# Performance work log

Measured on AMD Instinct MI355X. Metric: run time of the kernel, lower is better.

The kernel has to match this reference:

```python
import jax, jax.numpy as jnp
import numpy as np

NUM_GRAPHS = 512
LEAKY_SLOPE = 0.01


def _gconv(x, src, dst, w, W_root, W_rel, b_rel):
    # PyG GraphConv: out = lin_rel(sum_j w_ij * x_j) + lin_root(x)
    msg = x[src] * w[:, None]                       # [E, d] gather + scale
    agg = jax.ops.segment_sum(msg, dst, num_segments=x.shape[0])  # scatter-add
    return agg @ W_rel + b_rel + x @ W_root


def setup_inputs() -> dict:
    key = jax.random.key(0)
    ks = jax.random.split(key, 12)
    N, E, D, H, C = 100000, 1250000, 64, 64, 8
    x_embeddings = jax.random.normal(ks[0], (N, D), dtype=jnp.float32)
    edge_index = jax.random.randint(ks[1], (2, E), 0, N, dtype=jnp.int64)
    weights = jax.random.uniform(ks[2], (E,), dtype=jnp.float32)
    batch = jnp.sort(jax.random.randint(ks[3], (N,), 0, NUM_GRAPHS, dtype=jnp.int64))
    s1 = 1.0 / np.sqrt(D)
    s2 = 1.0 / np.sqrt(H)
    W1_root = jax.random.uniform(ks[4], (D, H), jnp.float32, -s1, s1)
    W1_rel = jax.random.uniform(ks[5], (D, H), jnp.float32, -s1, s1)
    b1 = jax.random.uniform(ks[6], (H,), jnp.float32, -s1, s1)
    W2_root = jax.random.uniform(ks[7], (H, H), jnp.float32, -s2, s2)
    W2_rel = jax.random.uniform(ks[8], (H, H), jnp.float32, -s2, s2)
    b2 = jax.random.uniform(ks[9], (H,), jnp.float32, -s2, s2)
    Wl_root = jax.random.uniform(ks[10], (H, C), jnp.float32, -s2, s2)
    bl = jax.random.uniform(ks[11], (C,), jnp.float32, -s2, s2)
    return {"x_embeddings": x_embeddings, "edge_index": edge_index,
            "weights": weights, "batch": batch,
            "W1_root": W1_root, "W1_rel": W1_rel, "b1": b1,
            "W2_root": W2_root, "W2_rel": W2_rel, "b2": b2,
            "Wl_root": Wl_root, "bl": bl}


def reference(x_embeddings, edge_index, weights, batch,
              W1_root, W1_rel, b1, W2_root, W2_rel, b2, Wl_root, bl):
    src, dst = edge_index[0], edge_index[1]
    x = _gconv(x_embeddings, src, dst, weights, W1_root, W1_rel, b1)
    x = jax.nn.leaky_relu(x, LEAKY_SLOPE)
    x = _gconv(x, src, dst, weights, W2_root, W2_rel, b2)
    x = jax.nn.leaky_relu(x, LEAKY_SLOPE)
    # global_mean_pool over graph ids
    summed = jax.ops.segment_sum(x, batch, num_segments=NUM_GRAPHS)
    counts = jax.ops.segment_sum(jnp.ones((x.shape[0],), x.dtype), batch,
                                 num_segments=NUM_GRAPHS)
    pooled = summed / jnp.maximum(counts, 1.0)[:, None]
    # final GraphConv applied with no edges: agg = 0 -> W_root x + b_rel
    out = pooled @ Wl_root + bl
    return out
```

## Files before the change

kernel.cpp:

```cpp
#include <hip/hip_runtime.h>

#define LEAKY_SLOPE 0.01f
#define NUM_GRAPHS 512
#define TILE 4096
#define NB_MAX 512
#define POOL_SPAN 8

typedef __attribute__((ext_vector_type(8))) short short8;
typedef __attribute__((ext_vector_type(4))) float f32x4;

static __device__ __forceinline__ unsigned short f2bf(float f) {
    unsigned u = __float_as_uint(f);
    u += 0x7FFFu + ((u >> 16) & 1u);
    return (unsigned short)(u >> 16);
}
static __device__ __forceinline__ float bf2f(unsigned short h) {
    return __uint_as_float(((unsigned)h) << 16);
}

static __device__ __forceinline__ int wave_incl_scan(int v, int lane) {
#pragma unroll
    for (int off = 1; off < 64; off <<= 1) {
        int t = __shfl_up(v, off, 64);
        if (lane >= off) v += t;
    }
    return v;
}

__global__ __launch_bounds__(256)
void hist_kernel(const int* __restrict__ dst, int* __restrict__ bucketCnt,
                 int E, int NB) {
    __shared__ int h[NB_MAX];
    for (int t = threadIdx.x; t < NB_MAX; t += 256) h[t] = 0;
    __syncthreads();
    const int base = blockIdx.x * TILE;
#pragma unroll
    for (int i = 0; i < TILE / 256; ++i) {
        int e = base + i * 256 + threadIdx.x;
        if (e < E) atomicAdd(&h[dst[e] >> 8], 1);
    }
    __syncthreads();
    for (int t = threadIdx.x; t < NB; t += 256)
        if (h[t]) atomicAdd(&bucketCnt[t], h[t]);
}

__global__ __launch_bounds__(512)
void bscan_kernel(const int* __restrict__ bucketCnt, int* __restrict__ bucketBase,
                  int* __restrict__ cursor, int* __restrict__ rowStart,
                  float* __restrict__ pooled, int N, int E, int NB) {
    __shared__ int ws[8];
    const int t = threadIdx.x, lane = t & 63, wid = t >> 6;
    int v = (t < NB) ? bucketCnt[t] : 0;
    int s = wave_incl_scan(v, lane);
    if (lane == 63) ws[wid] = s;
    __syncthreads();
    int add = 0;
    for (int i = 0; i < wid; ++i) add += ws[i];
    if (t < NB) {
        int excl = s + add - v;
        bucketBase[t] = excl;
        cursor[t] = excl;
    }
    if (t == 0) rowStart[N] = E;
    float4 z = make_float4(0.f, 0.f, 0.f, 0.f);
#pragma unroll
    for (int i = 0; i < 16; ++i)
        ((float4*)pooled)[t * 16 + i] = z;
}

__global__ __launch_bounds__(256)
void p1x_kernel(const int* __restrict__ src, const int* __restrict__ dst,
                const float* __restrict__ w, int* __restrict__ cursor,
                int2* __restrict__ tmp, int E, int NB, int histBlocks,
                const float* __restrict__ x, unsigned short* __restrict__ xB,
                int xElems, int xBlocks,
                const float* __restrict__ W1rel, const float* __restrict__ W1root,
                const float* __restrict__ W2rel, const float* __restrict__ W2root,
                unsigned short* __restrict__ Bt1, unsigned short* __restrict__ Bt2) {
    const int bid = blockIdx.x;
    if (bid < histBlocks) {
        __shared__ int h[NB_MAX];
        __shared__ int cur[NB_MAX];
        __shared__ int lstart[NB_MAX];
        __shared__ int gbase[NB_MAX];
        __shared__ int ws[4];
        __shared__ int2 pay[TILE];
        __shared__ unsigned short bk[TILE];

        for (int t = threadIdx.x; t < NB_MAX; t += 256) h[t] = 0;
        __syncthreads();

        const int base = bid * TILE;
        int   myb[TILE / 256];
        int   myp[TILE / 256];
        float myw[TILE / 256];
#pragma unroll
        for (int i = 0; i < TILE / 256; ++i) {
            int e = base + i * 256 + threadIdx.x;
            if (e < E) {
                int d = dst[e];
                myb[i] = d >> 8;
                myp[i] = src[e] | ((d & 255) << 20);
                myw[i] = w[e];
                atomicAdd(&h[myb[i]], 1);
            } else {
                myb[i] = -1;
            }
        }
        __syncthreads();

        {
            const int t = threadIdx.x, lane = t & 63, wid = t >> 6;
            int a = h[2 * t], b = h[2 * t + 1];
            int s = wave_incl_scan(a + b, lane);
            if (lane == 63) ws[wid] = s;
            __syncthreads();
            int add = 0;
            for (int i = 0; i < wid; ++i) add += ws[i];
            int excl = s + add - (a + b);
            lstart[2 * t] = excl;
            lstart[2 * t + 1] = excl + a;
            cur[2 * t] = excl;
            cur[2 * t + 1] = excl + a;
        }
        __syncthreads();

#pragma unroll
        for (int i = 0; i < TILE / 256; ++i) {
            if (myb[i] >= 0) {
                int p = atomicAdd(&cur[myb[i]], 1);
                pay[p] = make_int2(myp[i], __float_as_int(myw[i]));
                bk[p] = (unsigned short)myb[i];
            }
        }
        __syncthreads();

        for (int t = threadIdx.x; t < NB; t += 256) {
            int c = h[t];
            if (c) gbase[t] = atomicAdd(&cursor[t], c);
        }
        __syncthreads();

        const int total = min(TILE, E - base);
        for (int s2 = threadIdx.x; s2 < total; s2 += 256) {
            int b2 = bk[s2];
            tmp[gbase[b2] + s2 - lstart[b2]] = pay[s2];
        }
    } else if (bid < histBlocks + xBlocks) {
        int i = (bid - histBlocks) * 256 + threadIdx.x;
        if (i < xElems) {
            float4 f = ((const float4*)x)[i];
            ushort4 o = make_ushort4(f2bf(f.x), f2bf(f.y), f2bf(f.z), f2bf(f.w));
            ((ushort4*)xB)[i] = o;
        }
    } else {
        int b2 = bid - histBlocks - xBlocks;
        for (int idx = b2 * 2048 + threadIdx.x; idx < (b2 + 1) * 2048; idx += 256) {
            int which = idx >> 13;
            int j = idx & 8191;
            int n = j >> 7, k = j & 127;
            const float* Wr = which ? W2rel : W1rel;
            const float* Wo = which ? W2root : W1root;
            float v = (k < 64) ? Wr[k * 64 + n] : Wo[(k - 64) * 64 + n];
            (which ? Bt2 : Bt1)[j] = f2bf(v);
        }
    }
}

__global__ __launch_bounds__(512)
void p2_build(const int2* __restrict__ tmp, const int* __restrict__ bucketBase,
              int* __restrict__ rowStart, int2* __restrict__ edata,
              int N, int E, int NB) {
    const int b = blockIdx.x;
    const int s = bucketBase[b];
    const int e2 = (b + 1 < NB) ? bucketBase[b + 1] : E;
    __shared__ int h[256];
    __shared__ int cur[256];
    __shared__ int ws[8];
    if (threadIdx.x < 256) h[threadIdx.x] = 0;
    __syncthreads();
    for (int j = s + threadIdx.x; j < e2; j += 512) {
        int dl = (tmp[j].x >> 20) & 255;
        atomicAdd(&h[dl], 1);
    }
    __syncthreads();
    const int t = threadIdx.x, lane = t & 63, wid = t >> 6;
    int v = (t < 256) ? h[t] : 0;
    int sc = wave_incl_scan(v, lane);
    if (lane == 63) ws[wid] = sc;
    __syncthreads();
    int add = 0;
    for (int i = 0; i < wid; ++i) add += ws[i];
    int excl = sc + add - v;
    if (t < 256) {
        const int node = b * 256 + t;
        if (node < N) rowStart[node] = s + excl;
        cur[t] = excl;
    }
    __syncthreads();
    for (int j = s + threadIdx.x; j < e2; j += 512) {
        int2 v2 = tmp[j];
        int dl = (v2.x >> 20) & 255;
        int p = atomicAdd(&cur[dl], 1);
        edata[s + p] = make_int2(v2.x & 0x1FFFF, v2.y);
    }
}

template <int POOL>
__global__ __launch_bounds__(512)
void fused_layer(const unsigned short* __restrict__ xin,
                 const int* __restrict__ rowStart,
                 const int2* __restrict__ edata,
                 const unsigned short* __restrict__ Bt,
                 const float* __restrict__ bias,
                 unsigned short* __restrict__ xoutB,
                 const int* __restrict__ batch,
                 float* __restrict__ pooled, int N) {
    const int lane = threadIdx.x & 63;
    const int wave = threadIdx.x >> 6;
    const int grp  = lane >> 4;
    const int l16  = lane & 15;
    const int f4   = l16 * 4;
    const int m0   = (int)blockIdx.x * 32;

    __shared__ __align__(16) unsigned short aggL[32][72];
    __shared__ float lpool[POOL_SPAN * 64];

    int gmin = 0;
    if (POOL) {
        gmin = batch[m0 < N ? m0 : N - 1];
        for (int i = threadIdx.x; i < POOL_SPAN * 64; i += 512) lpool[i] = 0.f;
    }

    int rsv = 0;
    if (lane <= 32) {
        int rn = m0 + lane;
        rsv = rowStart[rn < N ? rn : N];
    }
#pragma unroll
    for (int p = 0; p < 2; ++p) {
        const int ia = (wave << 2) + (p << 1);
        const int sa = __shfl(rsv, ia, 64);
        const int ea = __shfl(rsv, ia + 1, 64);
        const int sb = ea;
        const int eb = __shfl(rsv, ia + 2, 64);

        float aA0 = 0.f, aA1 = 0.f, aA2 = 0.f, aA3 = 0.f;
        float aB0 = 0.f, aB1 = 0.f, aB2 = 0.f, aB3 = 0.f;
        int ja = sa, jb = sb;
        while (ja < ea || jb < eb) {
            const bool da = ja < ea;
            const bool db = jb < eb;
            int2 edA[4], edB[4];
            if (da) {
#pragma unroll
                for (int u = 0; u < 4; ++u) {
                    int ii = ja + u * 4 + grp;
                    edA[u] = edata[ii < ea ? ii : sa];
                }
            }
            if (db) {
#pragma unroll
                for (int u = 0; u < 4; ++u) {
                    int ii = jb + u * 4 + grp;
                    edB[u] = edata[ii < eb ? ii : sb];
                }
            }
            ushort4 rA[4], rB[4];
            if (da) {
#pragma unroll
                for (int u = 0; u < 4; ++u)
                    rA[u] = *(const ushort4*)(xin + (size_t)edA[u].x * 64 + f4);
            }
            if (db) {
#pragma unroll
                for (int u = 0; u < 4; ++u)
                    rB[u] = *(const ushort4*)(xin + (size_t)edB[u].x * 64 + f4);
            }
            if (da) {
#pragma unroll
                for (int u = 0; u < 4; ++u) {
                    float wv = (ja + u * 4 + grp < ea) ? __int_as_float(edA[u].y) : 0.0f;
                    aA0 += bf2f(rA[u].x) * wv;  aA1 += bf2f(rA[u].y) * wv;
                    aA2 += bf2f(rA[u].z) * wv;  aA3 += bf2f(rA[u].w) * wv;
                }
                ja += 16;
            }
            if (db) {
#pragma unroll
                for (int u = 0; u < 4; ++u) {
                    float wv = (jb + u * 4 + grp < eb) ? __int_as_float(edB[u].y) : 0.0f;
                    aB0 += bf2f(rB[u].x) * wv;  aB1 += bf2f(rB[u].y) * wv;
                    aB2 += bf2f(rB[u].z) * wv;  aB3 += bf2f(rB[u].w) * wv;
                }
                jb += 16;
            }
        }
        aA0 += __shfl_xor(aA0, 16, 64);  aA1 += __shfl_xor(aA1, 16, 64);
        aA2 += __shfl_xor(aA2, 16, 64);  aA3 += __shfl_xor(aA3, 16, 64);
        aA0 += __shfl_xor(aA0, 32, 64);  aA1 += __shfl_xor(aA1, 32, 64);
        aA2 += __shfl_xor(aA2, 32, 64);  aA3 += __shfl_xor(aA3, 32, 64);
        aB0 += __shfl_xor(aB0, 16, 64);  aB1 += __shfl_xor(aB1, 16, 64);
        aB2 += __shfl_xor(aB2, 16, 64);  aB3 += __shfl_xor(aB3, 16, 64);
        aB0 += __shfl_xor(aB0, 32, 64);  aB1 += __shfl_xor(aB1, 32, 64);
        aB2 += __shfl_xor(aB2, 32, 64);  aB3 += __shfl_xor(aB3, 32, 64);
        if (grp == 0) {
            *(ushort4*)(&aggL[ia][f4]) =
                make_ushort4(f2bf(aA0), f2bf(aA1), f2bf(aA2), f2bf(aA3));
            *(ushort4*)(&aggL[ia + 1][f4]) =
                make_ushort4(f2bf(aB0), f2bf(aB1), f2bf(aB2), f2bf(aB3));
        }
    }

    __syncthreads();

    {
        const int s = wave >> 2;
        const int t = wave & 3;
        short8 bf[4];
#pragma unroll
        for (int k = 0; k < 4; ++k)
            bf[k] = *(const short8*)(Bt + (t * 16 + l16) * 128 + k * 32 + grp * 8);

        f32x4 acc = (f32x4){0.f, 0.f, 0.f, 0.f};
        int row = m0 + s * 16 + l16;
        int rowc = row < N ? row : N - 1;
        const unsigned short* xrow = xin + (size_t)rowc * 64;
        short8 af[4];
        af[0] = *(const short8*)(&aggL[s * 16 + l16][grp * 8]);
        af[1] = *(const short8*)(&aggL[s * 16 + l16][32 + grp * 8]);
        af[2] = *(const short8*)(xrow + grp * 8);
        af[3] = *(const short8*)(xrow + 32 + grp * 8);
#pragma unroll
        for (int k = 0; k < 4; ++k) {
            if (POOL == 0)
                acc = __builtin_amdgcn_mfma_f32_16x16x32_bf16(bf[k], af[k], acc, 0, 0, 0);
            else
                acc = __builtin_amdgcn_mfma_f32_16x16x32_bf16(af[k], bf[k], acc, 0, 0, 0);
        }

        if (POOL == 0) {
            const int node = m0 + s * 16 + l16;
            if (node < N) {
                const float4 bb = *(const float4*)(bias + t * 16 + grp * 4);
                float v0 = acc[0] + bb.x;
                float v1 = acc[1] + bb.y;
                float v2 = acc[2] + bb.z;
                float v3 = acc[3] + bb.w;
                v0 = (v0 > 0.f) ? v0 : LEAKY_SLOPE * v0;
                v1 = (v1 > 0.f) ? v1 : LEAKY_SLOPE * v1;
                v2 = (v2 > 0.f) ? v2 : LEAKY_SLOPE * v2;
                v3 = (v3 > 0.f) ? v3 : LEAKY_SLOPE * v3;
                ushort4 o = make_ushort4(f2bf(v0), f2bf(v1), f2bf(v2), f2bf(v3));
                *(ushort4*)(xoutB + (size_t)node * 64 + t * 16 + grp * 4) = o;
            }
        } else {
            const int col = t * 16 + l16;
            const float b = bias[col];
            const int rowbase = m0 + s * 16 + grp * 4;
            float v[4]; int g[4]; int nv = 0;
#pragma unroll
            for (int r = 0; r < 4; ++r) {
                int row2 = rowbase + r;
                if (row2 < N) {
                    float a = acc[r] + b;
                    a = (a > 0.0f) ? a : LEAKY_SLOPE * a;
                    v[nv] = a;
                    g[nv] = batch[row2];
                    ++nv;
                }
            }
            if (nv == 4 && g[0] == g[3]) {
                int gl = g[0] - gmin;
                float sum = v[0] + v[1] + v[2] + v[3];
                if (gl < POOL_SPAN) atomicAdd(&lpool[gl * 64 + col], sum);
                else                atomicAdd(&pooled[g[0] * 64 + col], sum);
            } else {
                for (int r = 0; r < nv; ++r) {
                    int gl = g[r] - gmin;
                    if (gl < POOL_SPAN) atomicAdd(&lpool[gl * 64 + col], v[r]);
                    else                atomicAdd(&pooled[g[r] * 64 + col], v[r]);
                }
            }
        }
    }

    if (POOL) {
        __syncthreads();
        for (int i = threadIdx.x; i < POOL_SPAN * 64; i += 512) {
            float vv = lpool[i];
            if (vv != 0.0f)
                atomicAdd(&pooled[(gmin + (i >> 6)) * 64 + (i & 63)], vv);
        }
    }
}

__global__ __launch_bounds__(64)
void final_kernel(const float* __restrict__ pooled, const int* __restrict__ batch,
                  int N, const float* __restrict__ Wl, const float* __restrict__ bl,
                  float* __restrict__ out) {
    const int g = blockIdx.x;
    const int j = threadIdx.x;
    __shared__ float sp[64];
    __shared__ int scnt;
    if (j == 0) {
        int lo = 0, hi = N;
        while (lo < hi) { int mid = (lo + hi) >> 1; if (batch[mid] < g) lo = mid + 1; else hi = mid; }
        const int start = lo;
        hi = N;
        while (lo < hi) { int mid = (lo + hi) >> 1; if (batch[mid] < g + 1) lo = mid + 1; else hi = mid; }
        scnt = lo - start;
    }
    __syncthreads();
    const float c = fmaxf((float)scnt, 1.0f);
    sp[j] = pooled[g * 64 + j] / c;
    __syncthreads();
    if (j < 8) {
        float acc = bl[j];
#pragma unroll
        for (int k = 0; k < 64; ++k) acc += sp[k] * Wl[k * 8 + j];
        out[g * 8 + j] = acc;
    }
}

extern "C" void kernel_launch(void* const* d_in, const int* in_sizes, int n_in,
                              void* d_out, int out_size, void* d_ws, size_t ws_size,
                              hipStream_t stream) {
    const float* x      = (const float*)d_in[0];
    const int*   ei     = (const int*)  d_in[1];
    const float* w      = (const float*)d_in[2];
    const int*   batch  = (const int*)  d_in[3];
    const float* W1root = (const float*)d_in[4];
    const float* W1rel  = (const float*)d_in[5];
    const float* b1     = (const float*)d_in[6];
    const float* W2root = (const float*)d_in[7];
    const float* W2rel  = (const float*)d_in[8];
    const float* b2     = (const float*)d_in[9];
    const float* Wl     = (const float*)d_in[10];
    const float* bl     = (const float*)d_in[11];
    float* out = (float*)d_out;

    const int E = in_sizes[2];
    const int N = in_sizes[3];
    const int* src = ei;
    const int* dst = ei + E;
    const int NB = (N + 255) / 256;

    unsigned short* xB   = (unsigned short*)d_ws;
    unsigned short* aggB = xB   + (size_t)N * 64;
    unsigned short* x1B  = aggB + (size_t)N * 64;
    int2*  tmp      = (int2*)(x1B + (size_t)N * 64);
    int2*  edata    = tmp + E;
    unsigned short* Bt1 = (unsigned short*)(edata + E);
    unsigned short* Bt2 = Bt1 + 64 * 128;
    int*   rowStart = (int*)(Bt2 + 64 * 128);
    int*   bucketCnt  = rowStart + (N + 1);
    int*   bucketBase = bucketCnt + NB_MAX;
    int*   cursor     = bucketBase + NB_MAX;
    float* pooled   = (float*)(cursor + NB_MAX);
    (void)aggB;

    const int histBlocks = (E + TILE - 1) / TILE;
    const int xElems = N * 16;
    const int xBlocks = (xElems + 255) / 256;

    (void)hipMemsetAsync(bucketCnt, 0, NB_MAX * sizeof(int), stream);
    hist_kernel<<<histBlocks, 256, 0, stream>>>(dst, bucketCnt, E, NB);
    bscan_kernel<<<1, 512, 0, stream>>>(bucketCnt, bucketBase, cursor, rowStart,
                                        pooled, N, E, NB);
    p1x_kernel<<<histBlocks + xBlocks + 8, 256, 0, stream>>>(
        src, dst, w, cursor, tmp, E, NB, histBlocks,
        x, xB, xElems, xBlocks,
        W1rel, W1root, W2rel, W2root, Bt1, Bt2);
    p2_build<<<NB, 512, 0, stream>>>(tmp, bucketBase, rowStart, edata, N, E, NB);

    const int fBlocks = (N + 31) / 32;
    fused_layer<0><<<fBlocks, 512, 0, stream>>>(xB, rowStart, edata, Bt1, b1,
                                                x1B, nullptr, nullptr, N);
    fused_layer<1><<<fBlocks, 512, 0, stream>>>(x1B, rowStart, edata, Bt2, b2,
                                                nullptr, batch, pooled, N);
    final_kernel<<<NUM_GRAPHS, 64, 0, stream>>>(pooled, batch, N, Wl, bl, out);
}
```

Before: 274.8 us.

## Replace two-pass bucketed CSR build with global-atomic counting sort

Swaps the CSR construction, which used bucket histograms, a block-local shared-memory sort, a temp buffer and a per-bucket second pass, for a direct per-node atomic histogram, a three-kernel prefix scan, and a scatter using global atomics on per-node cursors. This removes the temp buffer and the second reorder pass over all edges. In exchange it relies on contended global atomics and uncoalesced scattered writes, and it adds extra kernel launches. Edge order within each row becomes nondeterministic, so floating-point sums may vary slightly between runs.

```diff
diff --git a/kernel.cpp b/kernel.cpp
--- a/kernel.cpp
+++ b/kernel.cpp
@@ -2,8 +2,6 @@
 
 #define LEAKY_SLOPE 0.01f
 #define NUM_GRAPHS 512
-#define TILE 4096
-#define NB_MAX 512
 #define POOL_SPAN 8
 
 typedef __attribute__((ext_vector_type(8))) short short8;
@@ -28,123 +26,20 @@
 }
 
 __global__ __launch_bounds__(256)
-void hist_kernel(const int* __restrict__ dst, int* __restrict__ bucketCnt,
-                 int E, int NB) {
-    __shared__ int h[NB_MAX];
-    for (int t = threadIdx.x; t < NB_MAX; t += 256) h[t] = 0;
-    __syncthreads();
-    const int base = blockIdx.x * TILE;
-#pragma unroll
-    for (int i = 0; i < TILE / 256; ++i) {
-        int e = base + i * 256 + threadIdx.x;
-        if (e < E) atomicAdd(&h[dst[e] >> 8], 1);
-    }
-    __syncthreads();
-    for (int t = threadIdx.x; t < NB; t += 256)
-        if (h[t]) atomicAdd(&bucketCnt[t], h[t]);
-}
-
-__global__ __launch_bounds__(512)
-void bscan_kernel(const int* __restrict__ bucketCnt, int* __restrict__ bucketBase,
-                  int* __restrict__ cursor, int* __restrict__ rowStart,
-                  float* __restrict__ pooled, int N, int E, int NB) {
-    __shared__ int ws[8];
-    const int t = threadIdx.x, lane = t & 63, wid = t >> 6;
-    int v = (t < NB) ? bucketCnt[t] : 0;
-    int s = wave_incl_scan(v, lane);
-    if (lane == 63) ws[wid] = s;
-    __syncthreads();
-    int add = 0;
-    for (int i = 0; i < wid; ++i) add += ws[i];
-    if (t < NB) {
-        int excl = s + add - v;
-        bucketBase[t] = excl;
-        cursor[t] = excl;
-    }
-    if (t == 0) rowStart[N] = E;
-    float4 z = make_float4(0.f, 0.f, 0.f, 0.f);
-#pragma unroll
-    for (int i = 0; i < 16; ++i)
-        ((float4*)pooled)[t * 16 + i] = z;
-}
-
-__global__ __launch_bounds__(256)
-void p1x_kernel(const int* __restrict__ src, const int* __restrict__ dst,
-                const float* __restrict__ w, int* __restrict__ cursor,
-                int2* __restrict__ tmp, int E, int NB, int histBlocks,
-                const float* __restrict__ x, unsigned short* __restrict__ xB,
-                int xElems, int xBlocks,
-                const float* __restrict__ W1rel, const float* __restrict__ W1root,
-                const float* __restrict__ W2rel, const float* __restrict__ W2root,
-                unsigned short* __restrict__ Bt1, unsigned short* __restrict__ Bt2) {
+void prep1_kernel(const int* __restrict__ dst, int* __restrict__ rowCnt,
+                  int E, int histBlocks,
+                  const float* __restrict__ x, unsigned short* __restrict__ xB,
+                  int xElems, int xBlocks,
+                  const float* __restrict__ W1rel, const float* __restrict__ W1root,
+                  const float* __restrict__ W2rel, const float* __restrict__ W2root,
+                  unsigned short* __restrict__ Bt1, unsigned short* __restrict__ Bt2) {
     const int bid = blockIdx.x;
     if (bid < histBlocks) {
-        __shared__ int h[NB_MAX];
-        __shared__ int cur[NB_MAX];
-        __shared__ int lstart[NB_MAX];
-        __shared__ int gbase[NB_MAX];
-        __shared__ int ws[4];
-        __shared__ int2 pay[TILE];
-        __shared__ unsigned short bk[TILE];
-
-        for (int t = threadIdx.x; t < NB_MAX; t += 256) h[t] = 0;
-        __syncthreads();
-
-        const int base = bid * TILE;
-        int   myb[TILE / 256];
-        int   myp[TILE / 256];
-        float myw[TILE / 256];
-#pragma unroll
-        for (int i = 0; i < TILE / 256; ++i) {
+        const int base = bid * 2048;
+#pragma unroll
+        for (int i = 0; i < 8; ++i) {
             int e = base + i * 256 + threadIdx.x;
-            if (e < E) {
-                int d = dst[e];
-                myb[i] = d >> 8;
-                myp[i] = src[e] | ((d & 255) << 20);
-                myw[i] = w[e];
-                atomicAdd(&h[myb[i]], 1);
-            } else {
-                myb[i] = -1;
-            }
-        }
-        __syncthreads();
-
-        {
-            const int t = threadIdx.x, lane = t & 63, wid = t >> 6;
-            int a = h[2 * t], b = h[2 * t + 1];
-            int s = wave_incl_scan(a + b, lane);
-            if (lane == 63) ws[wid] = s;
-            __syncthreads();
-            int add = 0;
-            for (int i = 0; i < wid; ++i) add += ws[i];
-            int excl = s + add - (a + b);
-            lstart[2 * t] = excl;
-            lstart[2 * t + 1] = excl + a;
-            cur[2 * t] = excl;
-            cur[2 * t + 1] = excl + a;
-        }
-        __syncthreads();
-
-#pragma unroll
-        for (int i = 0; i < TILE / 256; ++i) {
-            if (myb[i] >= 0) {
-                int p = atomicAdd(&cur[myb[i]], 1);
-                pay[p] = make_int2(myp[i], __float_as_int(myw[i]));
-                bk[p] = (unsigned short)myb[i];
-            }
-        }
-        __syncthreads();
-
-        for (int t = threadIdx.x; t < NB; t += 256) {
-            int c = h[t];
-            if (c) gbase[t] = atomicAdd(&cursor[t], c);
-        }
-        __syncthreads();
-
-        const int total = min(TILE, E - base);
-        for (int s2 = threadIdx.x; s2 < total; s2 += 256) {
-            int b2 = bk[s2];
-            tmp[gbase[b2] + s2 - lstart[b2]] = pay[s2];
+            if (e < E) atomicAdd(&rowCnt[dst[e]], 1);
         }
     } else if (bid < histBlocks + xBlocks) {
         int i = (bid - histBlocks) * 256 + threadIdx.x;
@@ -168,41 +63,65 @@
 }
 
 __global__ __launch_bounds__(512)
-void p2_build(const int2* __restrict__ tmp, const int* __restrict__ bucketBase,
-              int* __restrict__ rowStart, int2* __restrict__ edata,
-              int N, int E, int NB) {
+void scan1_kernel(const int* __restrict__ rowCnt, int* __restrict__ rowStart,
+                  int* __restrict__ blockSum, int N) {
+    __shared__ int ws[8];
+    const int b = blockIdx.x, t = threadIdx.x, lane = t & 63, wid = t >> 6;
+    const int i = b * 512 + t;
+    int v = (i < N) ? rowCnt[i] : 0;
+    int s = wave_incl_scan(v, lane);
+    if (lane == 63) ws[wid] = s;
+    __syncthreads();
+    int add = 0;
+    for (int k = 0; k < wid; ++k) add += ws[k];
+    int incl = s + add;
+    if (i < N) rowStart[i] = incl - v;
+    if (t == 511) blockSum[b] = incl;
+}
+
+__global__ __launch_bounds__(256)
+void scan2_kernel(int* __restrict__ blockSum, int nBlocks,
+                  int* __restrict__ rowStart, int N, int E) {
+    __shared__ int ws[4];
+    const int t = threadIdx.x, lane = t & 63, wid = t >> 6;
+    int v = (t < nBlocks) ? blockSum[t] : 0;
+    int s = wave_incl_scan(v, lane);
+    if (lane == 63) ws[wid] = s;
+    __syncthreads();
+    int add = 0;
+    for (int k = 0; k < wid; ++k) add += ws[k];
+    if (t < nBlocks) blockSum[t] = s + add - v;
+    if (t == 0) rowStart[N] = E;
+}
+
+__global__ __launch_bounds__(512)
+void scan3_kernel(int* __restrict__ rowStart, const int* __restrict__ blockSum,
+                  int* __restrict__ cursor, float* __restrict__ pooled, int N) {
     const int b = blockIdx.x;
-    const int s = bucketBase[b];
-    const int e2 = (b + 1 < NB) ? bucketBase[b + 1] : E;
-    __shared__ int h[256];
-    __shared__ int cur[256];
-    __shared__ int ws[8];
-    if (threadIdx.x < 256) h[threadIdx.x] = 0;
-    __syncthreads();
-    for (int j = s + threadIdx.x; j < e2; j += 512) {
-        int dl = (tmp[j].x >> 20) & 255;
-        atomicAdd(&h[dl], 1);
-    }
-    __syncthreads();
-    const int t = threadIdx.x, lane = t & 63, wid = t >> 6;
-    int v = (t < 256) ? h[t] : 0;
-    int sc = wave_incl_scan(v, lane);
-    if (lane == 63) ws[wid] = sc;
-    __syncthreads();
-    int add = 0;
-    for (int i = 0; i < wid; ++i) add += ws[i];
-    int excl = sc + add - v;
-    if (t < 256) {
-        const int node = b * 256 + t;
-        if (node < N) rowStart[node] = s + excl;
-        cur[t] = excl;
-    }
-    __syncthreads();
-    for (int j = s + threadIdx.x; j < e2; j += 512) {
-        int2 v2 = tmp[j];
-        int dl = (v2.x >> 20) & 255;
-        int p = atomicAdd(&cur[dl], 1);
-        edata[s + p] = make_int2(v2.x & 0x1FFFF, v2.y);
+    const int i = b * 512 + threadIdx.x;
+    if (i < N) {
+        int v = rowStart[i] + blockSum[b];
+        rowStart[i] = v;
+        cursor[i] = v;
+    }
+    const int tot = gridDim.x * 512;
+    for (int j = b * 512 + threadIdx.x; j < NUM_GRAPHS * 64; j += tot)
+        pooled[j] = 0.f;
+}
+
+__global__ __launch_bounds__(256)
+void scatter_kernel(const int* __restrict__ src, const int* __restrict__ dst,
+                    const float* __restrict__ w, int* __restrict__ cursor,
+                    int2* __restrict__ edata, int E) {
+    const int base = blockIdx.x * 2048;
+#pragma unroll
+    for (int i = 0; i < 8; ++i) {
+        int e = base + i * 256 + threadIdx.x;
+        if (e < E) {
+            int d = dst[e];
+            int p = atomicAdd(&cursor[d], 1);
+            edata[p] = make_int2(src[e], __float_as_int(w[e]));
+        }
     }
 }
 
@@ -444,35 +363,32 @@
     const int N = in_sizes[3];
     const int* src = ei;
     const int* dst = ei + E;
-    const int NB = (N + 255) / 256;
 
     unsigned short* xB   = (unsigned short*)d_ws;
-    unsigned short* aggB = xB   + (size_t)N * 64;
-    unsigned short* x1B  = aggB + (size_t)N * 64;
-    int2*  tmp      = (int2*)(x1B + (size_t)N * 64);
-    int2*  edata    = tmp + E;
+    unsigned short* x1B  = xB + (size_t)N * 64;
+    int2*  edata    = (int2*)(x1B + (size_t)N * 64);
     unsigned short* Bt1 = (unsigned short*)(edata + E);
     unsigned short* Bt2 = Bt1 + 64 * 128;
     int*   rowStart = (int*)(Bt2 + 64 * 128);
-    int*   bucketCnt  = rowStart + (N + 1);
-    int*   bucketBase = bucketCnt + NB_MAX;
-    int*   cursor     = bucketBase + NB_MAX;
-    float* pooled   = (float*)(cursor + NB_MAX);
-    (void)aggB;
-
-    const int histBlocks = (E + TILE - 1) / TILE;
+    int*   rowCnt   = rowStart + (N + 1);
+    int*   cursor   = rowCnt + N;
+    int*   blockSum = cursor + N;
+    float* pooled   = (float*)(blockSum + 256);
+
+    const int histBlocks = (E + 2047) / 2048;
     const int xElems = N * 16;
     const int xBlocks = (xElems + 255) / 256;
-
-    (void)hipMemsetAsync(bucketCnt, 0, NB_MAX * sizeof(int), stream);
-    hist_kernel<<<histBlocks, 256, 0, stream>>>(dst, bucketCnt, E, NB);
-    bscan_kernel<<<1, 512, 0, stream>>>(bucketCnt, bucketBase, cursor, rowStart,
-                                        pooled, N, E, NB);
-    p1x_kernel<<<histBlocks + xBlocks + 8, 256, 0, stream>>>(
-        src, dst, w, cursor, tmp, E, NB, histBlocks,
+    const int nScan = (N + 511) / 512;
+
+    (void)hipMemsetAsync(rowCnt, 0, (size_t)N * sizeof(int), stream);
+    prep1_kernel<<<histBlocks + xBlocks + 8, 256, 0, stream>>>(
+        dst, rowCnt, E, histBlocks,
         x, xB, xElems, xBlocks,
         W1rel, W1root, W2rel, W2root, Bt1, Bt2);
-    p2_build<<<NB, 512, 0, stream>>>(tmp, bucketBase, rowStart, edata, N, E, NB);
+    scan1_kernel<<<nScan, 512, 0, stream>>>(rowCnt, rowStart, blockSum, N);
+    scan2_kernel<<<1, 256, 0, stream>>>(blockSum, nScan, rowStart, N, E);
+    scan3_kernel<<<nScan, 512, 0, stream>>>(rowStart, blockSum, cursor, pooled, N);
+    scatter_kernel<<<histBlocks, 256, 0, stream>>>(src, dst, w, cursor, edata, E);
 
     const int fBlocks = (N + 31) / 32;
     fused_layer<0><<<fBlocks, 512, 0, stream>>>(xB, rowStart, edata, Bt1, b1,
```

New measurement: 385.7 us. 1.4x slower.

## Replace histogram pre-pass with fixed-capacity bucket segments for edge binning

Applied to the files above, without the earlier changes.

Removes the separate histogram kernel, its memset and the first scan. Each 256-node bucket now gets a fixed segment of SEG slots in the temp buffer, with its cursor starting at t*SEG, so binning needs no prior counts. A small scan over the final cursor values then yields the compacted bucket bases for CSR building. This saves one full pass over dst and two launches. The risk is that a bucket receiving more than SEG edges would overflow into its neighbour; with ~3125 expected edges per bucket that is unlikely for these inputs but not guaranteed in general.

```diff
diff --git a/kernel.cpp b/kernel.cpp
--- a/kernel.cpp
+++ b/kernel.cpp
@@ -4,6 +4,7 @@
 #define NUM_GRAPHS 512
 #define TILE 4096
 #define NB_MAX 512
+#define SEG 4096
 #define POOL_SPAN 8
 
 typedef __attribute__((ext_vector_type(8))) short short8;
@@ -27,41 +28,10 @@
     return v;
 }
 
-__global__ __launch_bounds__(256)
-void hist_kernel(const int* __restrict__ dst, int* __restrict__ bucketCnt,
-                 int E, int NB) {
-    __shared__ int h[NB_MAX];
-    for (int t = threadIdx.x; t < NB_MAX; t += 256) h[t] = 0;
-    __syncthreads();
-    const int base = blockIdx.x * TILE;
-#pragma unroll
-    for (int i = 0; i < TILE / 256; ++i) {
-        int e = base + i * 256 + threadIdx.x;
-        if (e < E) atomicAdd(&h[dst[e] >> 8], 1);
-    }
-    __syncthreads();
-    for (int t = threadIdx.x; t < NB; t += 256)
-        if (h[t]) atomicAdd(&bucketCnt[t], h[t]);
-}
-
 __global__ __launch_bounds__(512)
-void bscan_kernel(const int* __restrict__ bucketCnt, int* __restrict__ bucketBase,
-                  int* __restrict__ cursor, int* __restrict__ rowStart,
-                  float* __restrict__ pooled, int N, int E, int NB) {
-    __shared__ int ws[8];
-    const int t = threadIdx.x, lane = t & 63, wid = t >> 6;
-    int v = (t < NB) ? bucketCnt[t] : 0;
-    int s = wave_incl_scan(v, lane);
-    if (lane == 63) ws[wid] = s;
-    __syncthreads();
-    int add = 0;
-    for (int i = 0; i < wid; ++i) add += ws[i];
-    if (t < NB) {
-        int excl = s + add - v;
-        bucketBase[t] = excl;
-        cursor[t] = excl;
-    }
-    if (t == 0) rowStart[N] = E;
+void curinit_kernel(int* __restrict__ cursor, float* __restrict__ pooled, int NB) {
+    const int t = threadIdx.x;
+    if (t < NB) cursor[t] = t * SEG;
     float4 z = make_float4(0.f, 0.f, 0.f, 0.f);
 #pragma unroll
     for (int i = 0; i < 16; ++i)
@@ -168,19 +138,35 @@
 }
 
 __global__ __launch_bounds__(512)
+void bscan2_kernel(const int* __restrict__ cursor, int* __restrict__ bucketBase,
+                   int* __restrict__ rowStart, int N, int E, int NB) {
+    __shared__ int ws[8];
+    const int t = threadIdx.x, lane = t & 63, wid = t >> 6;
+    int v = (t < NB) ? (cursor[t] - t * SEG) : 0;
+    int s = wave_incl_scan(v, lane);
+    if (lane == 63) ws[wid] = s;
+    __syncthreads();
+    int add = 0;
+    for (int i = 0; i < wid; ++i) add += ws[i];
+    if (t < NB) bucketBase[t] = s + add - v;
+    if (t == 0) rowStart[N] = E;
+}
+
+__global__ __launch_bounds__(512)
 void p2_build(const int2* __restrict__ tmp, const int* __restrict__ bucketBase,
               int* __restrict__ rowStart, int2* __restrict__ edata,
               int N, int E, int NB) {
     const int b = blockIdx.x;
-    const int s = bucketBase[b];
-    const int e2 = (b + 1 < NB) ? bucketBase[b + 1] : E;
+    const int sOut = bucketBase[b];
+    const int cnt  = ((b + 1 < NB) ? bucketBase[b + 1] : E) - sOut;
+    const int sIn  = b * SEG;
     __shared__ int h[256];
     __shared__ int cur[256];
     __shared__ int ws[8];
     if (threadIdx.x < 256) h[threadIdx.x] = 0;
     __syncthreads();
-    for (int j = s + threadIdx.x; j < e2; j += 512) {
-        int dl = (tmp[j].x >> 20) & 255;
+    for (int j = threadIdx.x; j < cnt; j += 512) {
+        int dl = (tmp[sIn + j].x >> 20) & 255;
         atomicAdd(&h[dl], 1);
     }
     __syncthreads();
@@ -194,15 +180,15 @@
     int excl = sc + add - v;
     if (t < 256) {
         const int node = b * 256 + t;
-        if (node < N) rowStart[node] = s + excl;
+        if (node < N) rowStart[node] = sOut + excl;
         cur[t] = excl;
     }
     __syncthreads();
-    for (int j = s + threadIdx.x; j < e2; j += 512) {
-        int2 v2 = tmp[j];
+    for (int j = threadIdx.x; j < cnt; j += 512) {
+        int2 v2 = tmp[sIn + j];
         int dl = (v2.x >> 20) & 255;
         int p = atomicAdd(&cur[dl], 1);
-        edata[s + p] = make_int2(v2.x & 0x1FFFF, v2.y);
+        edata[sOut + p] = make_int2(v2.x & 0x1FFFF, v2.y);
     }
 }
 
@@ -447,31 +433,26 @@
     const int NB = (N + 255) / 256;
 
     unsigned short* xB   = (unsigned short*)d_ws;
-    unsigned short* aggB = xB   + (size_t)N * 64;
-    unsigned short* x1B  = aggB + (size_t)N * 64;
+    unsigned short* x1B  = xB + (size_t)N * 64;
     int2*  tmp      = (int2*)(x1B + (size_t)N * 64);
-    int2*  edata    = tmp + E;
+    int2*  edata    = tmp + (size_t)NB_MAX * SEG;
     unsigned short* Bt1 = (unsigned short*)(edata + E);
     unsigned short* Bt2 = Bt1 + 64 * 128;
     int*   rowStart = (int*)(Bt2 + 64 * 128);
-    int*   bucketCnt  = rowStart + (N + 1);
-    int*   bucketBase = bucketCnt + NB_MAX;
+    int*   bucketBase = rowStart + (N + 1);
     int*   cursor     = bucketBase + NB_MAX;
     float* pooled   = (float*)(cursor + NB_MAX);
-    (void)aggB;
 
     const int histBlocks = (E + TILE - 1) / TILE;
     const int xElems = N * 16;
     const int xBlocks = (xElems + 255) / 256;
 
-    (void)hipMemsetAsync(bucketCnt, 0, NB_MAX * sizeof(int), stream);
-    hist_kernel<<<histBlocks, 256, 0, stream>>>(dst, bucketCnt, E, NB);
-    bscan_kernel<<<1, 512, 0, stream>>>(bucketCnt, bucketBase, cursor, rowStart,
-                                        pooled, N, E, NB);
+    curinit_kernel<<<1, 512, 0, stream>>>(cursor, pooled, NB);
     p1x_kernel<<<histBlocks + xBlocks + 8, 256, 0, stream>>>(
         src, dst, w, cursor, tmp, E, NB, histBlocks,
         x, xB, xElems, xBlocks,
         W1rel, W1root, W2rel, W2root, Bt1, Bt2);
+    bscan2_kernel<<<1, 512, 0, stream>>>(cursor, bucketBase, rowStart, N, E, NB);
     p2_build<<<NB, 512, 0, stream>>>(tmp, bucketBase, rowStart, edata, N, E, NB);
 
     const int fBlocks = (N + 31) / 32;
```

After: 257.8 us. 1.07x faster.
